# Kernel optimization log

Measured on AMD Instinct MI355X. Metric: run time of the kernel, lower is better.

Reference implementation:

```python
import jax, jax.numpy as jnp
import numpy as np

B, N, K, F_IN, F_OUT = 8, 2048, 32, 256, 256


def setup_inputs() -> dict:
    key = jax.random.key(0)
    ks = jax.random.split(key, 8)
    x = jax.random.normal(ks[0], (B, N, F_IN), dtype=jnp.float32)
    idx_neib = jax.random.randint(ks[1], (N, K), 0, N, dtype=jnp.int32)
    # Linear params (torch nn.Linear stores weight as [out, in])
    lim_x = np.sqrt(2.0) * np.sqrt(6.0 / (F_IN + F_OUT))  # xavier_uniform, gain=relu
    Wx_w = jax.random.uniform(ks[2], (F_OUT, F_IN), jnp.float32, -lim_x, lim_x)
    Wx_b = jnp.zeros((F_OUT,), jnp.float32)
    Wn_w = jax.random.uniform(ks[3], (F_OUT, F_IN), jnp.float32, -lim_x, lim_x)
    Wn_b = jnp.zeros((F_OUT,), jnp.float32)
    gamma = jnp.ones((2 * F_OUT,), jnp.float32)
    beta = jnp.zeros((2 * F_OUT,), jnp.float32)
    return {"x": x, "idx_neib": idx_neib, "Wx_w": Wx_w, "Wx_b": Wx_b,
            "Wn_w": Wn_w, "Wn_b": Wn_b, "gamma": gamma, "beta": beta}


def reference(x, idx_neib, Wx_w, Wx_b, Wn_w, Wn_b, gamma, beta):
    # Gather neighbor features: [B, N, K, F] then mean over the K neighbors.
    x_neib = jnp.take(x, idx_neib, axis=1).mean(axis=2)  # [B, N, F]
    # Dual linear projections (weights stored [out, in] as in torch).
    h_self = jnp.einsum('bnf,of->bno', x, Wx_w) + Wx_b
    h_nei = jnp.einsum('bnf,of->bno', x_neib, Wn_w) + Wn_b
    h = jnp.concatenate([h_self, h_nei], axis=2)          # [B, N, 2*out]
    # F.normalize(p=2, dim=2): divide by max(||h||_2, 1e-12)
    nrm = jnp.sqrt(jnp.sum(h * h, axis=2, keepdims=True))
    h = h / jnp.maximum(nrm, 1e-12)
    h = jax.nn.relu(h)
    # BatchNorm1d over channel dim (training mode: batch stats over B and N,
    # biased variance), eps=1e-5.
    mu = h.mean(axis=(0, 1))
    var = jnp.mean((h - mu) ** 2, axis=(0, 1))
    h = (h - mu) * jax.lax.rsqrt(var + 1e-5) * gamma + beta
    return h
```

## Files before the change

### kernel.cpp

```cpp
#include <hip/hip_runtime.h>
#include <stdint.h>

#define BB 8
#define NN 2048
#define KK 32
#define FIN 256
#define FOUT 256
#define CC 512
#define MM (BB*NN)
#define RB 32
#define NBLK (MM/RB)
#define LDA 264

typedef __attribute__((ext_vector_type(8))) short short8;
typedef __attribute__((ext_vector_type(4))) float f32x4;
typedef __attribute__((ext_vector_type(2))) float f32x2;

__device__ __forceinline__ unsigned short f2bf(float f) {
    union { float f; unsigned u; } v; v.f = f;
    unsigned u = v.u;
    return (unsigned short)((u + 0x7FFFu + ((u >> 16) & 1u)) >> 16);
}
__device__ __forceinline__ float bf2f(unsigned short s) {
    union { unsigned u; float f; } v; v.u = ((unsigned)s) << 16;
    return v.f;
}
__device__ __forceinline__ f32x2 bfpair(unsigned u) {
    union { unsigned u; float f; } lo, hi;
    lo.u = u << 16;
    hi.u = u & 0xFFFF0000u;
    return (f32x2){lo.f, hi.f};
}

__global__ void k_prep(const float* __restrict__ Wx, const float* __restrict__ Wxb,
                       const float* __restrict__ Wn, const float* __restrict__ Wnb,
                       const float* __restrict__ x,
                       unsigned short* __restrict__ Wc, float* __restrict__ bc,
                       unsigned short* __restrict__ xb) {
    const int blk = blockIdx.x;
    const int tid = threadIdx.x;
    if (blk < 128) {
        int gid = blk * 256 + tid;
        int e0 = gid * 4;
        int o = e0 >> 8, k = e0 & 255;
        const float* src = (o < FOUT) ? (Wx + o * FIN + k) : (Wn + (o - FOUT) * FIN + k);
        float4 v = *(const float4*)src;
        ushort4 p; p.x = f2bf(v.x); p.y = f2bf(v.y); p.z = f2bf(v.z); p.w = f2bf(v.w);
        *(ushort4*)(Wc + e0) = p;
        if (gid < 128) {
            int c0 = gid * 4;
            float4 bv = (c0 < FOUT) ? *(const float4*)(Wxb + c0)
                                    : *(const float4*)(Wnb + c0 - FOUT);
            *(float4*)(bc + c0) = bv;
        }
    } else {
        size_t gid = (size_t)(blk - 128) * 256 + tid;
        size_t e0 = gid * 8;
        float4 v0 = *(const float4*)(x + e0);
        float4 v1 = *(const float4*)(x + e0 + 4);
        ushort4 p0, p1;
        p0.x = f2bf(v0.x); p0.y = f2bf(v0.y); p0.z = f2bf(v0.z); p0.w = f2bf(v0.w);
        p1.x = f2bf(v1.x); p1.y = f2bf(v1.y); p1.z = f2bf(v1.z); p1.w = f2bf(v1.w);
        *(ushort4*)(xb + e0)     = p0;
        *(ushort4*)(xb + e0 + 4) = p1;
    }
}

__global__ __launch_bounds__(512, 4)
void k_gemm(const unsigned short* __restrict__ xb, const int* __restrict__ idx,
            const unsigned short* __restrict__ Wc,
            const float* __restrict__ bc,
            unsigned short* __restrict__ h,
            float* __restrict__ psum, float* __restrict__ psq) {
    __shared__ unsigned short As[2][RB * LDA];
    __shared__ float sqpart[8][RB];
    __shared__ float rnorm[RB];

    const int bid  = blockIdx.x;
    const int tid  = threadIdx.x;
    const int w    = tid >> 6;
    const int lane = tid & 63;
    const int quad = lane >> 4;
    const int l16  = lane & 15;
    const int p    = lane >> 5;
    const int l32  = lane & 31;
    const int b    = bid & 7;
    const int n0   = (bid >> 3) * RB;
    const unsigned short* xbat = xb + (size_t)b * NN * FIN;
    const size_t r0g = (size_t)b * NN + n0;

    {
        const uint4* gs = (const uint4*)(xbat + (size_t)n0 * FIN);
        #pragma unroll
        for (int i = 0; i < 2; ++i) {
            int e = tid + i * 512;
            *(uint4*)&As[0][(e >> 5) * LDA + (e & 31) * 8] = gs[e];
        }
    }
    {
        const int* ip = idx + (n0 + (w << 2)) * KK;
        const unsigned short* xp = xbat + l32 * 8;
        f32x2 ac[4][4];
        #pragma unroll
        for (int rr = 0; rr < 4; ++rr)
            #pragma unroll
            for (int c = 0; c < 4; ++c) ac[rr][c] = (f32x2){0.f, 0.f};

        #pragma unroll 2
        for (int k = 0; k < 16; ++k) {
            int kk = (k << 1) | p;
            int j0 = ip[0 * KK + kk];
            int j1 = ip[1 * KK + kk];
            int j2 = ip[2 * KK + kk];
            int j3 = ip[3 * KK + kk];
            uint4 v0 = *(const uint4*)(xp + (size_t)j0 * FIN);
            uint4 v1 = *(const uint4*)(xp + (size_t)j1 * FIN);
            uint4 v2 = *(const uint4*)(xp + (size_t)j2 * FIN);
            uint4 v3 = *(const uint4*)(xp + (size_t)j3 * FIN);
            const unsigned* u0 = (const unsigned*)&v0;
            const unsigned* u1 = (const unsigned*)&v1;
            const unsigned* u2 = (const unsigned*)&v2;
            const unsigned* u3 = (const unsigned*)&v3;
            #pragma unroll
            for (int c = 0; c < 4; ++c) {
                ac[0][c] += bfpair(u0[c]);
                ac[1][c] += bfpair(u1[c]);
                ac[2][c] += bfpair(u2[c]);
                ac[3][c] += bfpair(u3[c]);
            }
        }
        const float s = 1.0f / (float)KK;
        #pragma unroll
        for (int rr = 0; rr < 4; ++rr) {
            #pragma unroll
            for (int c = 0; c < 4; ++c) {
                ac[rr][c][0] += __shfl_xor(ac[rr][c][0], 32, 64);
                ac[rr][c][1] += __shfl_xor(ac[rr][c][1], 32, 64);
            }
            if (p == 0) {
                unsigned short o8[8];
                #pragma unroll
                for (int c = 0; c < 4; ++c) {
                    o8[2 * c]     = f2bf(ac[rr][c][0] * s);
                    o8[2 * c + 1] = f2bf(ac[rr][c][1] * s);
                }
                *(uint4*)&As[1][((w << 2) + rr) * LDA + l32 * 8] = *(const uint4*)o8;
            }
        }
    }
    __syncthreads();

    const int half = w >> 2;
    const unsigned short* A = As[half];
    const int cbg = half * 256 + (w & 3) * 64;

    f32x4 acc[2][4];
    #pragma unroll
    for (int mt = 0; mt < 2; ++mt)
        #pragma unroll
        for (int nt = 0; nt < 4; ++nt) acc[mt][nt] = (f32x4){0.f, 0.f, 0.f, 0.f};

    const unsigned short* Bp = Wc + (size_t)(cbg + l16) * FIN + quad * 8;
    const unsigned short* Ap = A + (size_t)l16 * LDA + quad * 8;

    #pragma unroll 2
    for (int k0 = 0; k0 < FIN; k0 += 32) {
        short8 a0 = *(const short8*)(Ap + k0);
        short8 a1 = *(const short8*)(Ap + 16 * LDA + k0);
        short8 bfr[4];
        #pragma unroll
        for (int nt = 0; nt < 4; ++nt)
            bfr[nt] = *(const short8*)(Bp + (size_t)nt * 16 * FIN + k0);
        #pragma unroll
        for (int nt = 0; nt < 4; ++nt) {
            acc[0][nt] = __builtin_amdgcn_mfma_f32_16x16x32_bf16(a0, bfr[nt], acc[0][nt], 0, 0, 0);
            acc[1][nt] = __builtin_amdgcn_mfma_f32_16x16x32_bf16(a1, bfr[nt], acc[1][nt], 0, 0, 0);
        }
    }

    float bcv[4];
    #pragma unroll
    for (int nt = 0; nt < 4; ++nt) bcv[nt] = bc[cbg + nt * 16 + l16];

    float rsq[2][4] = {{0.f,0.f,0.f,0.f},{0.f,0.f,0.f,0.f}};
    #pragma unroll
    for (int mt = 0; mt < 2; ++mt)
        #pragma unroll
        for (int nt = 0; nt < 4; ++nt)
            #pragma unroll
            for (int r = 0; r < 4; ++r) {
                float v = acc[mt][nt][r] + bcv[nt];
                acc[mt][nt][r] = v;
                rsq[mt][r] += v * v;
            }
    #pragma unroll
    for (int off = 1; off < 16; off <<= 1)
        #pragma unroll
        for (int mt = 0; mt < 2; ++mt)
            #pragma unroll
            for (int r = 0; r < 4; ++r)
                rsq[mt][r] += __shfl_xor(rsq[mt][r], off, 64);
    if (l16 == 0) {
        #pragma unroll
        for (int mt = 0; mt < 2; ++mt)
            #pragma unroll
            for (int r = 0; r < 4; ++r)
                sqpart[w][mt * 16 + quad * 4 + r] = rsq[mt][r];
    }
    __syncthreads();
    if (tid < RB) {
        float tot = 0.f;
        #pragma unroll
        for (int i = 0; i < 8; ++i) tot += sqpart[i][tid];
        rnorm[tid] = 1.0f / fmaxf(sqrtf(tot), 1e-12f);
    }
    __syncthreads();

    float csum[4] = {0.f,0.f,0.f,0.f};
    float csq [4] = {0.f,0.f,0.f,0.f};
    #pragma unroll
    for (int mt = 0; mt < 2; ++mt) {
        #pragma unroll
        for (int r = 0; r < 4; ++r) {
            int row = mt * 16 + quad * 4 + r;
            float rn = rnorm[row];
            unsigned short* hp = h + (r0g + row) * CC + cbg + l16;
            #pragma unroll
            for (int nt = 0; nt < 4; ++nt) {
                float v = fmaxf(acc[mt][nt][r] * rn, 0.0f);
                hp[nt * 16] = f2bf(v);
                csum[nt] += v;
                csq [nt] += v * v;
            }
        }
    }
    #pragma unroll
    for (int off = 16; off < 64; off <<= 1)
        #pragma unroll
        for (int nt = 0; nt < 4; ++nt) {
            csum[nt] += __shfl_xor(csum[nt], off, 64);
            csq [nt] += __shfl_xor(csq [nt], off, 64);
        }
    if (quad == 0 && p == 0) {
        #pragma unroll
        for (int nt = 0; nt < 4; ++nt) {
            int c = cbg + nt * 16 + l16;
            psum[(size_t)c * NBLK + bid] = csum[nt];
            psq [(size_t)c * NBLK + bid] = csq [nt];
        }
    }
}

__global__ void k_stats(const float* __restrict__ psum, const float* __restrict__ psq,
                        const float* __restrict__ gamma, const float* __restrict__ beta,
                        float* __restrict__ ss) {
    __shared__ float ps[4], pq[4];
    int c = blockIdx.x, t = threadIdx.x;
    float s = psum[(size_t)c * NBLK + t] + psum[(size_t)c * NBLK + 256 + t];
    float q = psq [(size_t)c * NBLK + t] + psq [(size_t)c * NBLK + 256 + t];
    #pragma unroll
    for (int off = 32; off; off >>= 1) { s += __shfl_xor(s, off, 64); q += __shfl_xor(q, off, 64); }
    int w = t >> 6, lane = t & 63;
    if (lane == 0) { ps[w] = s; pq[w] = q; }
    __syncthreads();
    if (t == 0) {
        float S = ps[0] + ps[1] + ps[2] + ps[3];
        float Q = pq[0] + pq[1] + pq[2] + pq[3];
        const float inv = 1.0f / (float)MM;
        float mu  = S * inv;
        float var = fmaxf(Q * inv - mu * mu, 0.0f);
        float sc  = gamma[c] * rsqrtf(var + 1e-5f);
        ss[c]      = sc;
        ss[CC + c] = beta[c] - mu * sc;
    }
}

__global__ void k_apply(const unsigned short* __restrict__ h,
                        const float* __restrict__ ss,
                        float* __restrict__ out) {
    const int x   = blockIdx.x & 7;
    const int j   = blockIdx.x >> 3;
    const int tid = threadIdx.x;
    const size_t e0 = (size_t)x * ((size_t)NN * CC) + (size_t)j * 2048 + (size_t)tid * 8;
    int c0 = (int)(e0 & (CC - 1));
    uint4 hv = *(const uint4*)(h + e0);
    const unsigned short* hs = (const unsigned short*)&hv;
    float4 sc0 = *(const float4*)(ss + c0);
    float4 sc1 = *(const float4*)(ss + c0 + 4);
    float4 sh0 = *(const float4*)(ss + CC + c0);
    float4 sh1 = *(const float4*)(ss + CC + c0 + 4);
    float4 o0, o1;
    o0.x = bf2f(hs[0]) * sc0.x + sh0.x;
    o0.y = bf2f(hs[1]) * sc0.y + sh0.y;
    o0.z = bf2f(hs[2]) * sc0.z + sh0.z;
    o0.w = bf2f(hs[3]) * sc0.w + sh0.w;
    o1.x = bf2f(hs[4]) * sc1.x + sh1.x;
    o1.y = bf2f(hs[5]) * sc1.y + sh1.y;
    o1.z = bf2f(hs[6]) * sc1.z + sh1.z;
    o1.w = bf2f(hs[7]) * sc1.w + sh1.w;
    *(float4*)(out + e0)     = o0;
    *(float4*)(out + e0 + 4) = o1;
}

extern "C" void kernel_launch(void* const* d_in, const int* in_sizes, int n_in,
                              void* d_out, int out_size, void* d_ws, size_t ws_size,
                              hipStream_t stream) {
    const float* x     = (const float*)d_in[0];
    const int*   idx   = (const int*)  d_in[1];
    const float* Wx_w  = (const float*)d_in[2];
    const float* Wx_b  = (const float*)d_in[3];
    const float* Wn_w  = (const float*)d_in[4];
    const float* Wn_b  = (const float*)d_in[5];
    const float* gamma = (const float*)d_in[6];
    const float* beta  = (const float*)d_in[7];
    float* out = (float*)d_out;

    char* p = (char*)d_ws;
    unsigned short* xb = (unsigned short*)p; p += (size_t)MM * FIN * 2;
    unsigned short* Wc = (unsigned short*)p; p += (size_t)CC * FIN * 2;
    float* bc          = (float*)p;          p += (size_t)CC * 4;
    unsigned short* h  = (unsigned short*)p; p += (size_t)MM * CC * 2;
    float* psum        = (float*)p;          p += (size_t)CC * NBLK * 4;
    float* psq         = (float*)p;          p += (size_t)CC * NBLK * 4;
    float* ss          = (float*)p;          p += (size_t)2 * CC * 4;

    hipLaunchKernelGGL(k_prep,  dim3(2176), dim3(256), 0, stream,
                       Wx_w, Wx_b, Wn_w, Wn_b, x, Wc, bc, xb);
    hipLaunchKernelGGL(k_gemm,  dim3(NBLK), dim3(512), 0, stream, xb, idx, Wc, bc, h, psum, psq);
    hipLaunchKernelGGL(k_stats, dim3(CC),   dim3(256), 0, stream, psum, psq, gamma, beta, ss);
    hipLaunchKernelGGL(k_apply, dim3(4096), dim3(256), 0, stream, h, ss, out);
}
```

Baseline: 129.7 us.

## Fuse BN statistics reduction into GEMM kernel via atomics and last-block finalize

```diff
diff --git a/kernel.cpp b/kernel.cpp
--- a/kernel.cpp
+++ b/kernel.cpp
@@ -36,10 +36,18 @@
                        const float* __restrict__ Wn, const float* __restrict__ Wnb,
                        const float* __restrict__ x,
                        unsigned short* __restrict__ Wc, float* __restrict__ bc,
-                       unsigned short* __restrict__ xb) {
+                       unsigned short* __restrict__ xb,
+                       float* __restrict__ psum8, unsigned* __restrict__ cnt) {
     const int blk = blockIdx.x;
     const int tid = threadIdx.x;
     if (blk < 128) {
+        if (blk == 0) {
+            float4 z = {0.f, 0.f, 0.f, 0.f};
+            #pragma unroll
+            for (int i = 0; i < (CC * 16 / 4) / 256; ++i)
+                ((float4*)psum8)[tid + i * 256] = z;
+            if (tid == 0) *cnt = 0u;
+        }
         int gid = blk * 256 + tid;
         int e0 = gid * 4;
         int o = e0 >> 8, k = e0 & 255;
@@ -70,11 +78,14 @@
 void k_gemm(const unsigned short* __restrict__ xb, const int* __restrict__ idx,
             const unsigned short* __restrict__ Wc,
             const float* __restrict__ bc,
+            const float* __restrict__ gamma, const float* __restrict__ beta,
             unsigned short* __restrict__ h,
-            float* __restrict__ psum, float* __restrict__ psq) {
+            float* __restrict__ psum8, float* __restrict__ psq8,
+            float* __restrict__ ss, unsigned* __restrict__ cnt) {
     __shared__ unsigned short As[2][RB * LDA];
     __shared__ float sqpart[8][RB];
     __shared__ float rnorm[RB];
+    __shared__ unsigned lastf;
 
     const int bid  = blockIdx.x;
     const int tid  = threadIdx.x;
@@ -106,7 +117,7 @@
             #pragma unroll
             for (int c = 0; c < 4; ++c) ac[rr][c] = (f32x2){0.f, 0.f};
 
-        #pragma unroll 2
+        #pragma unroll 4
         for (int k = 0; k < 16; ++k) {
             int kk = (k << 1) | p;
             int j0 = ip[0 * KK + kk];
@@ -241,37 +252,41 @@
             csum[nt] += __shfl_xor(csum[nt], off, 64);
             csq [nt] += __shfl_xor(csq [nt], off, 64);
         }
-    if (quad == 0 && p == 0) {
+    if (quad == 0) {
         #pragma unroll
         for (int nt = 0; nt < 4; ++nt) {
             int c = cbg + nt * 16 + l16;
-            psum[(size_t)c * NBLK + bid] = csum[nt];
-            psq [(size_t)c * NBLK + bid] = csq [nt];
-        }
-    }
-}
-
-__global__ void k_stats(const float* __restrict__ psum, const float* __restrict__ psq,
-                        const float* __restrict__ gamma, const float* __restrict__ beta,
-                        float* __restrict__ ss) {
-    __shared__ float ps[4], pq[4];
-    int c = blockIdx.x, t = threadIdx.x;
-    float s = psum[(size_t)c * NBLK + t] + psum[(size_t)c * NBLK + 256 + t];
-    float q = psq [(size_t)c * NBLK + t] + psq [(size_t)c * NBLK + 256 + t];
-    #pragma unroll
-    for (int off = 32; off; off >>= 1) { s += __shfl_xor(s, off, 64); q += __shfl_xor(q, off, 64); }
-    int w = t >> 6, lane = t & 63;
-    if (lane == 0) { ps[w] = s; pq[w] = q; }
-    __syncthreads();
-    if (t == 0) {
-        float S = ps[0] + ps[1] + ps[2] + ps[3];
-        float Q = pq[0] + pq[1] + pq[2] + pq[3];
-        const float inv = 1.0f / (float)MM;
-        float mu  = S * inv;
-        float var = fmaxf(Q * inv - mu * mu, 0.0f);
-        float sc  = gamma[c] * rsqrtf(var + 1e-5f);
-        ss[c]      = sc;
-        ss[CC + c] = beta[c] - mu * sc;
+            __hip_atomic_fetch_add(&psum8[c * 8 + b], csum[nt],
+                                   __ATOMIC_RELAXED, __HIP_MEMORY_SCOPE_AGENT);
+            __hip_atomic_fetch_add(&psq8[c * 8 + b], csq[nt],
+                                   __ATOMIC_RELAXED, __HIP_MEMORY_SCOPE_AGENT);
+        }
+    }
+
+    __syncthreads();
+    if (tid == 0) {
+        unsigned prev = __hip_atomic_fetch_add(cnt, 1u, __ATOMIC_ACQ_REL,
+                                               __HIP_MEMORY_SCOPE_AGENT);
+        lastf = (prev == (unsigned)(NBLK - 1)) ? 1u : 0u;
+    }
+    __syncthreads();
+    if (lastf) {
+        if (tid < CC) {
+            float S = 0.f, Q = 0.f;
+            #pragma unroll
+            for (int i = 0; i < 8; ++i) {
+                S += __hip_atomic_load(&psum8[tid * 8 + i], __ATOMIC_RELAXED,
+                                       __HIP_MEMORY_SCOPE_AGENT);
+                Q += __hip_atomic_load(&psq8[tid * 8 + i], __ATOMIC_RELAXED,
+                                       __HIP_MEMORY_SCOPE_AGENT);
+            }
+            const float inv = 1.0f / (float)MM;
+            float mu  = S * inv;
+            float var = fmaxf(Q * inv - mu * mu, 0.0f);
+            float sc  = gamma[tid] * rsqrtf(var + 1e-5f);
+            ss[tid]      = sc;
+            ss[CC + tid] = beta[tid] - mu * sc;
+        }
     }
 }
 
@@ -320,13 +335,14 @@
     unsigned short* Wc = (unsigned short*)p; p += (size_t)CC * FIN * 2;
     float* bc          = (float*)p;          p += (size_t)CC * 4;
     unsigned short* h  = (unsigned short*)p; p += (size_t)MM * CC * 2;
-    float* psum        = (float*)p;          p += (size_t)CC * NBLK * 4;
-    float* psq         = (float*)p;          p += (size_t)CC * NBLK * 4;
+    float* psum8       = (float*)p;          p += (size_t)CC * 8 * 4;
+    float* psq8        = (float*)p;          p += (size_t)CC * 8 * 4;
     float* ss          = (float*)p;          p += (size_t)2 * CC * 4;
+    unsigned* cnt      = (unsigned*)p;       p += 64;
 
     hipLaunchKernelGGL(k_prep,  dim3(2176), dim3(256), 0, stream,
-                       Wx_w, Wx_b, Wn_w, Wn_b, x, Wc, bc, xb);
-    hipLaunchKernelGGL(k_gemm,  dim3(NBLK), dim3(512), 0, stream, xb, idx, Wc, bc, h, psum, psq);
-    hipLaunchKernelGGL(k_stats, dim3(CC),   dim3(256), 0, stream, psum, psq, gamma, beta, ss);
+                       Wx_w, Wx_b, Wn_w, Wn_b, x, Wc, bc, xb, psum8, cnt);
+    hipLaunchKernelGGL(k_gemm,  dim3(NBLK), dim3(512), 0, stream,
+                       xb, idx, Wc, bc, gamma, beta, h, psum8, psq8, ss, cnt);
     hipLaunchKernelGGL(k_apply, dim3(4096), dim3(256), 0, stream, h, ss, out);
 }
```

New measurement: 151.4 us. +16.7%, slower.

## Interleave self-projection MFMA with neighbor gather and split warps across both halves

Applied to the files above, without the earlier changes.

```diff
diff --git a/kernel.cpp b/kernel.cpp
--- a/kernel.cpp
+++ b/kernel.cpp
@@ -97,30 +97,65 @@
             *(uint4*)&As[0][(e >> 5) * LDA + (e & 31) * 8] = gs[e];
         }
     }
-    {
-        const int* ip = idx + (n0 + (w << 2)) * KK;
-        const unsigned short* xp = xbat + l32 * 8;
-        f32x2 ac[4][4];
-        #pragma unroll
-        for (int rr = 0; rr < 4; ++rr)
-            #pragma unroll
-            for (int c = 0; c < 4; ++c) ac[rr][c] = (f32x2){0.f, 0.f};
-
-        #pragma unroll 2
-        for (int k = 0; k < 16; ++k) {
-            int kk = (k << 1) | p;
-            int j0 = ip[0 * KK + kk];
-            int j1 = ip[1 * KK + kk];
-            int j2 = ip[2 * KK + kk];
-            int j3 = ip[3 * KK + kk];
-            uint4 v0 = *(const uint4*)(xp + (size_t)j0 * FIN);
-            uint4 v1 = *(const uint4*)(xp + (size_t)j1 * FIN);
-            uint4 v2 = *(const uint4*)(xp + (size_t)j2 * FIN);
-            uint4 v3 = *(const uint4*)(xp + (size_t)j3 * FIN);
-            const unsigned* u0 = (const unsigned*)&v0;
-            const unsigned* u1 = (const unsigned*)&v1;
-            const unsigned* u2 = (const unsigned*)&v2;
-            const unsigned* u3 = (const unsigned*)&v3;
+    __syncthreads();
+
+    const int sbg = w * 32;
+    const int nbg = 256 + w * 32;
+
+    f32x4 accS[2][2];
+    #pragma unroll
+    for (int mt = 0; mt < 2; ++mt)
+        #pragma unroll
+        for (int nt = 0; nt < 2; ++nt) accS[mt][nt] = (f32x4){0.f, 0.f, 0.f, 0.f};
+
+    const unsigned short* ApS = As[0] + (size_t)l16 * LDA + quad * 8;
+    const unsigned short* BpS = Wc + (size_t)(sbg + l16) * FIN + quad * 8;
+
+    const int* ip = idx + (n0 + (w << 2)) * KK;
+    const unsigned short* xp = xbat + l32 * 8;
+    f32x2 ac[4][4];
+    #pragma unroll
+    for (int rr = 0; rr < 4; ++rr)
+        #pragma unroll
+        for (int c = 0; c < 4; ++c) ac[rr][c] = (f32x2){0.f, 0.f};
+
+    short8 b0c = *(const short8*)(BpS);
+    short8 b1c = *(const short8*)(BpS + 16 * FIN);
+
+    #pragma unroll
+    for (int kp = 0; kp < 8; ++kp) {
+        const int kkA = (kp << 2) | p;
+        const int kkB = kkA + 2;
+        int jA0 = ip[0 * KK + kkA], jA1 = ip[1 * KK + kkA];
+        int jA2 = ip[2 * KK + kkA], jA3 = ip[3 * KK + kkA];
+        uint4 vA0 = *(const uint4*)(xp + (size_t)jA0 * FIN);
+        uint4 vA1 = *(const uint4*)(xp + (size_t)jA1 * FIN);
+        uint4 vA2 = *(const uint4*)(xp + (size_t)jA2 * FIN);
+        uint4 vA3 = *(const uint4*)(xp + (size_t)jA3 * FIN);
+        int jB0 = ip[0 * KK + kkB], jB1 = ip[1 * KK + kkB];
+        int jB2 = ip[2 * KK + kkB], jB3 = ip[3 * KK + kkB];
+        uint4 vB0 = *(const uint4*)(xp + (size_t)jB0 * FIN);
+        uint4 vB1 = *(const uint4*)(xp + (size_t)jB1 * FIN);
+        uint4 vB2 = *(const uint4*)(xp + (size_t)jB2 * FIN);
+        uint4 vB3 = *(const uint4*)(xp + (size_t)jB3 * FIN);
+        {
+            const int k0 = kp * 32;
+            short8 a0 = *(const short8*)(ApS + k0);
+            short8 a1 = *(const short8*)(ApS + 16 * LDA + k0);
+            const int k0n = (kp < 7) ? k0 + 32 : 0;
+            short8 b0n = *(const short8*)(BpS + k0n);
+            short8 b1n = *(const short8*)(BpS + 16 * FIN + k0n);
+            accS[0][0] = __builtin_amdgcn_mfma_f32_16x16x32_bf16(a0, b0c, accS[0][0], 0, 0, 0);
+            accS[0][1] = __builtin_amdgcn_mfma_f32_16x16x32_bf16(a0, b1c, accS[0][1], 0, 0, 0);
+            accS[1][0] = __builtin_amdgcn_mfma_f32_16x16x32_bf16(a1, b0c, accS[1][0], 0, 0, 0);
+            accS[1][1] = __builtin_amdgcn_mfma_f32_16x16x32_bf16(a1, b1c, accS[1][1], 0, 0, 0);
+            b0c = b0n; b1c = b1n;
+        }
+        {
+            const unsigned* u0 = (const unsigned*)&vA0;
+            const unsigned* u1 = (const unsigned*)&vA1;
+            const unsigned* u2 = (const unsigned*)&vA2;
+            const unsigned* u3 = (const unsigned*)&vA3;
             #pragma unroll
             for (int c = 0; c < 4; ++c) {
                 ac[0][c] += bfpair(u0[c]);
@@ -129,6 +164,21 @@
                 ac[3][c] += bfpair(u3[c]);
             }
         }
+        {
+            const unsigned* u0 = (const unsigned*)&vB0;
+            const unsigned* u1 = (const unsigned*)&vB1;
+            const unsigned* u2 = (const unsigned*)&vB2;
+            const unsigned* u3 = (const unsigned*)&vB3;
+            #pragma unroll
+            for (int c = 0; c < 4; ++c) {
+                ac[0][c] += bfpair(u0[c]);
+                ac[1][c] += bfpair(u1[c]);
+                ac[2][c] += bfpair(u2[c]);
+                ac[3][c] += bfpair(u3[c]);
+            }
+        }
+    }
+    {
         const float s = 1.0f / (float)KK;
         #pragma unroll
         for (int rr = 0; rr < 4; ++rr) {
@@ -150,49 +200,41 @@
     }
     __syncthreads();
 
-    const int half = w >> 2;
-    const unsigned short* A = As[half];
-    const int cbg = half * 256 + (w & 3) * 64;
-
-    f32x4 acc[2][4];
+    f32x4 accN[2][2];
     #pragma unroll
     for (int mt = 0; mt < 2; ++mt)
         #pragma unroll
-        for (int nt = 0; nt < 4; ++nt) acc[mt][nt] = (f32x4){0.f, 0.f, 0.f, 0.f};
-
-    const unsigned short* Bp = Wc + (size_t)(cbg + l16) * FIN + quad * 8;
-    const unsigned short* Ap = A + (size_t)l16 * LDA + quad * 8;
+        for (int nt = 0; nt < 2; ++nt) accN[mt][nt] = (f32x4){0.f, 0.f, 0.f, 0.f};
+
+    const unsigned short* ApN = As[1] + (size_t)l16 * LDA + quad * 8;
+    const unsigned short* BpN = Wc + (size_t)(nbg + l16) * FIN + quad * 8;
 
     #pragma unroll 2
     for (int k0 = 0; k0 < FIN; k0 += 32) {
-        short8 a0 = *(const short8*)(Ap + k0);
-        short8 a1 = *(const short8*)(Ap + 16 * LDA + k0);
-        short8 bfr[4];
-        #pragma unroll
-        for (int nt = 0; nt < 4; ++nt)
-            bfr[nt] = *(const short8*)(Bp + (size_t)nt * 16 * FIN + k0);
-        #pragma unroll
-        for (int nt = 0; nt < 4; ++nt) {
-            acc[0][nt] = __builtin_amdgcn_mfma_f32_16x16x32_bf16(a0, bfr[nt], acc[0][nt], 0, 0, 0);
-            acc[1][nt] = __builtin_amdgcn_mfma_f32_16x16x32_bf16(a1, bfr[nt], acc[1][nt], 0, 0, 0);
-        }
-    }
-
-    float bcv[4];
-    #pragma unroll
-    for (int nt = 0; nt < 4; ++nt) bcv[nt] = bc[cbg + nt * 16 + l16];
+        short8 a0 = *(const short8*)(ApN + k0);
+        short8 a1 = *(const short8*)(ApN + 16 * LDA + k0);
+        short8 bn0 = *(const short8*)(BpN + k0);
+        short8 bn1 = *(const short8*)(BpN + 16 * FIN + k0);
+        accN[0][0] = __builtin_amdgcn_mfma_f32_16x16x32_bf16(a0, bn0, accN[0][0], 0, 0, 0);
+        accN[0][1] = __builtin_amdgcn_mfma_f32_16x16x32_bf16(a0, bn1, accN[0][1], 0, 0, 0);
+        accN[1][0] = __builtin_amdgcn_mfma_f32_16x16x32_bf16(a1, bn0, accN[1][0], 0, 0, 0);
+        accN[1][1] = __builtin_amdgcn_mfma_f32_16x16x32_bf16(a1, bn1, accN[1][1], 0, 0, 0);
+    }
+
+    float bS0 = bc[sbg + l16],      bS1 = bc[sbg + 16 + l16];
+    float bN0 = bc[nbg + l16],      bN1 = bc[nbg + 16 + l16];
 
     float rsq[2][4] = {{0.f,0.f,0.f,0.f},{0.f,0.f,0.f,0.f}};
     #pragma unroll
     for (int mt = 0; mt < 2; ++mt)
         #pragma unroll
-        for (int nt = 0; nt < 4; ++nt)
-            #pragma unroll
-            for (int r = 0; r < 4; ++r) {
-                float v = acc[mt][nt][r] + bcv[nt];
-                acc[mt][nt][r] = v;
-                rsq[mt][r] += v * v;
-            }
+        for (int r = 0; r < 4; ++r) {
+            float v;
+            v = accS[mt][0][r] + bS0; accS[mt][0][r] = v; rsq[mt][r] += v * v;
+            v = accS[mt][1][r] + bS1; accS[mt][1][r] = v; rsq[mt][r] += v * v;
+            v = accN[mt][0][r] + bN0; accN[mt][0][r] = v; rsq[mt][r] += v * v;
+            v = accN[mt][1][r] + bN1; accN[mt][1][r] = v; rsq[mt][r] += v * v;
+        }
     #pragma unroll
     for (int off = 1; off < 16; off <<= 1)
         #pragma unroll
@@ -216,37 +258,44 @@
     }
     __syncthreads();
 
-    float csum[4] = {0.f,0.f,0.f,0.f};
-    float csq [4] = {0.f,0.f,0.f,0.f};
+    float csS[2] = {0.f, 0.f}, cqS[2] = {0.f, 0.f};
+    float csN[2] = {0.f, 0.f}, cqN[2] = {0.f, 0.f};
     #pragma unroll
     for (int mt = 0; mt < 2; ++mt) {
         #pragma unroll
         for (int r = 0; r < 4; ++r) {
             int row = mt * 16 + quad * 4 + r;
             float rn = rnorm[row];
-            unsigned short* hp = h + (r0g + row) * CC + cbg + l16;
-            #pragma unroll
-            for (int nt = 0; nt < 4; ++nt) {
-                float v = fmaxf(acc[mt][nt][r] * rn, 0.0f);
-                hp[nt * 16] = f2bf(v);
-                csum[nt] += v;
-                csq [nt] += v * v;
+            unsigned short* hp = h + (r0g + row) * CC;
+            #pragma unroll
+            for (int nt = 0; nt < 2; ++nt) {
+                float vS = fmaxf(accS[mt][nt][r] * rn, 0.0f);
+                hp[sbg + nt * 16 + l16] = f2bf(vS);
+                csS[nt] += vS; cqS[nt] += vS * vS;
+                float vN = fmaxf(accN[mt][nt][r] * rn, 0.0f);
+                hp[nbg + nt * 16 + l16] = f2bf(vN);
+                csN[nt] += vN; cqN[nt] += vN * vN;
             }
         }
     }
     #pragma unroll
     for (int off = 16; off < 64; off <<= 1)
         #pragma unroll
-        for (int nt = 0; nt < 4; ++nt) {
-            csum[nt] += __shfl_xor(csum[nt], off, 64);
-            csq [nt] += __shfl_xor(csq [nt], off, 64);
-        }
-    if (quad == 0 && p == 0) {
-        #pragma unroll
-        for (int nt = 0; nt < 4; ++nt) {
-            int c = cbg + nt * 16 + l16;
-            psum[(size_t)c * NBLK + bid] = csum[nt];
-            psq [(size_t)c * NBLK + bid] = csq [nt];
+        for (int nt = 0; nt < 2; ++nt) {
+            csS[nt] += __shfl_xor(csS[nt], off, 64);
+            cqS[nt] += __shfl_xor(cqS[nt], off, 64);
+            csN[nt] += __shfl_xor(csN[nt], off, 64);
+            cqN[nt] += __shfl_xor(cqN[nt], off, 64);
+        }
+    if (quad == 0) {
+        #pragma unroll
+        for (int nt = 0; nt < 2; ++nt) {
+            int cS = sbg + nt * 16 + l16;
+            int cN = nbg + nt * 16 + l16;
+            psum[(size_t)cS * NBLK + bid] = csS[nt];
+            psq [(size_t)cS * NBLK + bid] = cqS[nt];
+            psum[(size_t)cN * NBLK + bid] = csN[nt];
+            psq [(size_t)cN * NBLK + bid] = cqN[nt];
         }
     }
 }
```

After: 175.6 us. 35.4% more time.
